# Optimization experiments

Hardware: AMD Instinct MI355X
Metric: run time of the kernel (lower is better)

The kernel has to match this reference:

```python
import jax, jax.numpy as jnp
import numpy as np

N_NODES = 100000
N_EDGES = 600000
D_IN = 128
D_HID = 128
D_OUT = 128


def setup_inputs() -> dict:
    key = jax.random.key(0)
    k = jax.random.split(key, 6)
    x = jax.random.normal(k[0], (N_NODES, D_IN), dtype=jnp.float32)
    edge_index = jax.random.randint(k[1], (2, N_EDGES), 0, N_NODES, dtype=jnp.int64)
    # GCNConv params: glorot-ish weights, zero-init biases (randn-scaled here)
    W1 = jax.random.normal(k[2], (D_IN, D_HID), dtype=jnp.float32) / np.sqrt(D_IN)
    b1 = jnp.zeros((D_HID,), dtype=jnp.float32)
    W2 = jax.random.normal(k[3], (D_HID, D_OUT), dtype=jnp.float32) / np.sqrt(D_HID)
    b2 = jnp.zeros((D_OUT,), dtype=jnp.float32)
    return {"x": x, "edge_index": edge_index, "W1": W1, "b1": b1, "W2": W2, "b2": b2}


def _gcn_conv(x, W, b, src, dst, deg_inv_sqrt, n_nodes):
    # PyG GCNConv: h = x @ W; out_i = sum_{j->i} d_j^{-1/2} d_i^{-1/2} h_j + b
    h = x @ W  # [N, Dout]
    norm = (deg_inv_sqrt[src] * deg_inv_sqrt[dst])[:, None]  # [E, 1]
    msg = h[src] * norm  # gather: [E, Dout]
    out = jax.ops.segment_sum(msg, dst, num_segments=n_nodes)  # scatter-add
    return out + b


def reference(x, edge_index, W1, b1, W2, b2):
    n = x.shape[0]
    # add self loops
    loops = jnp.arange(n, dtype=edge_index.dtype)
    src = jnp.concatenate([edge_index[0], loops])
    dst = jnp.concatenate([edge_index[1], loops])
    # symmetric normalization degrees (computed on dst, deg >= 1 due to self loops)
    deg = jax.ops.segment_sum(jnp.ones_like(dst, dtype=x.dtype), dst, num_segments=n)
    deg_inv_sqrt = jax.lax.rsqrt(deg)
    h = _gcn_conv(x, W1, b1, src, dst, deg_inv_sqrt, n)
    h = jax.nn.relu(h)  # dropout is identity in eval mode
    out = _gcn_conv(h, W2, b2, src, dst, deg_inv_sqrt, n)
    return out
```

## Files before the change

### kernel.cpp

```cpp
#include <hip/hip_runtime.h>

#define D 128

typedef __attribute__((ext_vector_type(8))) short bf16x8;
typedef __attribute__((ext_vector_type(4))) float f32x4;
typedef __attribute__((ext_vector_type(4))) unsigned u32x4;

__device__ inline unsigned short f2bf(float f) {
    unsigned u = __builtin_bit_cast(unsigned, f);
    u += 0x7FFFu + ((u >> 16) & 1u);
    return (unsigned short)(u >> 16);
}
__device__ inline float bf_lo(unsigned u) { return __builtin_bit_cast(float, u << 16); }
__device__ inline float bf_hi(unsigned u) { return __builtin_bit_cast(float, u & 0xFFFF0000u); }

__global__ __launch_bounds__(256) void k_pack_zero(const float* __restrict__ W1,
                                                   const float* __restrict__ W2,
                                                   unsigned short* __restrict__ wp,
                                                   int* __restrict__ counts, int n) {
    if (blockIdx.x < 16) {
        const int t = blockIdx.x * 256 + threadIdx.x;
        const float* W = (t < 2048) ? W1 : W2;
        const int tt = t & 2047;
        const int lane = tt & 63;
        const int frag = tt >> 6;
        const int ct = frag >> 2;
        const int kk = frag & 3;
        const int col16 = lane & 15;
        const int kgrp = lane >> 4;
        bf16x8 d;
#pragma unroll
        for (int e = 0; e < 8; ++e)
            d[e] = (short)f2bf(W[(kk * 32 + kgrp * 8 + e) * D + ct * 16 + col16]);
        *reinterpret_cast<bf16x8*>(wp + (size_t)t * 8) = d;
    } else {
        const int i = (blockIdx.x - 16) * 256 + threadIdx.x;
        if (i < n) counts[i] = 0;
    }
}

__global__ void k_hist_rank(const int* __restrict__ dst, int* __restrict__ counts,
                            int* __restrict__ rank, int nE) {
    int e4 = (blockIdx.x * blockDim.x + threadIdx.x) * 4;
    if (e4 + 4 <= nE) {
        const int4 d = *reinterpret_cast<const int4*>(dst + e4);
        int4 r;
        r.x = atomicAdd(&counts[d.x], 1);
        r.y = atomicAdd(&counts[d.y], 1);
        r.z = atomicAdd(&counts[d.z], 1);
        r.w = atomicAdd(&counts[d.w], 1);
        *reinterpret_cast<int4*>(rank + e4) = r;
    } else {
        for (int e = e4; e < nE; ++e) rank[e] = atomicAdd(&counts[dst[e]], 1);
    }
}

__global__ __launch_bounds__(256) void k_scan_part(const int* __restrict__ counts,
                                                   int* __restrict__ bsum,
                                                   float* __restrict__ dis, int n) {
    const int t = threadIdx.x;
    const int base = blockIdx.x * 1024 + t * 4;
    int4 c = make_int4(0, 0, 0, 0);
    if (base + 4 <= n) {
        c = *reinterpret_cast<const int4*>(counts + base);
        float4 dv;
        dv.x = rsqrtf((float)(c.x + 1));
        dv.y = rsqrtf((float)(c.y + 1));
        dv.z = rsqrtf((float)(c.z + 1));
        dv.w = rsqrtf((float)(c.w + 1));
        *reinterpret_cast<float4*>(dis + base) = dv;
    } else if (base < n) {
        int cc[4] = {0, 0, 0, 0};
        for (int k = 0; k < 4; ++k)
            if (base + k < n) {
                cc[k] = counts[base + k];
                dis[base + k] = rsqrtf((float)(cc[k] + 1));
            }
        c.x = cc[0]; c.y = cc[1]; c.z = cc[2]; c.w = cc[3];
    }
    __shared__ int red[256];
    red[t] = c.x + c.y + c.z + c.w;
    __syncthreads();
    for (int off = 128; off > 0; off >>= 1) {
        if (t < off) red[t] += red[t + off];
        __syncthreads();
    }
    if (t == 0) bsum[blockIdx.x] = red[0];
}

__global__ __launch_bounds__(256) void k_scan_final(const int* __restrict__ counts,
                                                    const int* __restrict__ bsum,
                                                    int* __restrict__ starts, int n, int nB) {
    __shared__ int sb[128];
    __shared__ int ts[256];
    const int t = threadIdx.x;
    const int b = blockIdx.x;

    if (t < 128) sb[t] = (t < nB) ? bsum[t] : 0;
    __syncthreads();
    for (int off = 1; off < 128; off <<= 1) {
        int add = (t < 128 && t >= off) ? sb[t - off] : 0;
        __syncthreads();
        if (t < 128) sb[t] += add;
        __syncthreads();
    }
    const int block_off = (b > 0) ? sb[b - 1] : 0;

    const int base = b * 1024 + t * 4;
    int4 c = make_int4(0, 0, 0, 0);
    if (base + 4 <= n) {
        c = *reinterpret_cast<const int4*>(counts + base);
    } else if (base < n) {
        if (base + 0 < n) c.x = counts[base + 0];
        if (base + 1 < n) c.y = counts[base + 1];
        if (base + 2 < n) c.z = counts[base + 2];
    }
    const int s = c.x + c.y + c.z + c.w;
    ts[t] = s;
    __syncthreads();
    for (int off = 1; off < 256; off <<= 1) {
        int add = (t >= off) ? ts[t - off] : 0;
        __syncthreads();
        ts[t] += add;
        __syncthreads();
    }
    int excl = block_off + ts[t] - s;

    int4 w;
    w.x = excl;
    w.y = w.x + c.x;
    w.z = w.y + c.y;
    w.w = w.z + c.z;
    if (base + 4 <= n) {
        *reinterpret_cast<int4*>(starts + base) = w;
    } else if (base < n) {
        if (base + 0 < n) starts[base + 0] = w.x;
        if (base + 1 < n) starts[base + 1] = w.y;
        if (base + 2 < n) starts[base + 2] = w.z;
    }
    if (b == 0 && t == 0) starts[n] = sb[nB - 1];
}

__global__ __launch_bounds__(256, 3) void k_scatter_gemm(const int* __restrict__ src,
                                                         const int* __restrict__ dst,
                                                         const int* __restrict__ rank,
                                                         const int* __restrict__ starts,
                                                         int* __restrict__ esrc, int nE, int nsc,
                                                         const float* __restrict__ X,
                                                         const unsigned short* __restrict__ wp,
                                                         const float* __restrict__ dis,
                                                         unsigned short* __restrict__ outbf,
                                                         int n) {
    __shared__ __align__(16) unsigned short At[64 * 128];
    if (blockIdx.x < nsc) {
        int e4 = (blockIdx.x * blockDim.x + threadIdx.x) * 4;
        if (e4 + 4 <= nE) {
            const int4 s = *reinterpret_cast<const int4*>(src + e4);
            const int4 d = *reinterpret_cast<const int4*>(dst + e4);
            const int4 r = *reinterpret_cast<const int4*>(rank + e4);
            esrc[starts[d.x] + r.x] = s.x;
            esrc[starts[d.y] + r.y] = s.y;
            esrc[starts[d.z] + r.z] = s.z;
            esrc[starts[d.w] + r.w] = s.w;
        } else {
            for (int e = e4; e < nE; ++e)
                esrc[starts[dst[e]] + rank[e]] = src[e];
        }
        return;
    }
    const int st = blockIdx.x - nsc;
    const int tid = threadIdx.x;
    const int lane = tid & 63;
    const int wv = tid >> 6;
    const int col16 = lane & 15;
    const int kgrp = lane >> 4;

    float4 pf[8];
#pragma unroll
    for (int c = 0; c < 4; ++c) {
        const int idx = c * 2048 + tid * 8;
        const int row = idx >> 7;
        const int col = idx & 127;
        int grow = st * 64 + row;
        if (grow >= n) grow = n - 1;
        const float4* p = reinterpret_cast<const float4*>(X + (size_t)grow * D + col);
        pf[2 * c] = p[0];
        pf[2 * c + 1] = p[1];
    }
#pragma unroll
    for (int c = 0; c < 4; ++c) {
        const int idx = c * 2048 + tid * 8;
        const int row = idx >> 7;
        const int col = idx & 127;
        const float4 f0 = pf[2 * c], f1 = pf[2 * c + 1];
        float v[8] = {f0.x, f0.y, f0.z, f0.w, f1.x, f1.y, f1.z, f1.w};
        bf16x8 d;
#pragma unroll
        for (int e = 0; e < 8; ++e) d[e] = (short)f2bf(v[e]);
        const int waddr = row * 128 + (col ^ ((row & 7) << 3));
        *reinterpret_cast<bf16x8*>(&At[waddr]) = d;
    }
    __syncthreads();

    bf16x8 a[4];
#pragma unroll
    for (int kk = 0; kk < 4; ++kk) {
        const int raddr = (wv * 16 + col16) * 128 +
                          ((kk * 32 + kgrp * 8) ^ ((col16 & 7) << 3));
        a[kk] = *reinterpret_cast<const bf16x8*>(&At[raddr]);
    }

    const int node = st * 64 + wv * 16 + col16;
    const float dn = (node < n) ? dis[node] : 0.0f;
    unsigned short* op = outbf + (size_t)node * D + kgrp * 4;

#pragma unroll
    for (int h = 0; h < 2; ++h) {
        bf16x8 bw[4][4];
#pragma unroll
        for (int c2 = 0; c2 < 4; ++c2)
#pragma unroll
            for (int kk = 0; kk < 4; ++kk)
                bw[c2][kk] = *reinterpret_cast<const bf16x8*>(
                        wp + (size_t)(((h * 4 + c2) * 4 + kk) * 64 + lane) * 8);

        f32x4 acc[4];
#pragma unroll
        for (int c2 = 0; c2 < 4; ++c2) acc[c2] = (f32x4){0.f, 0.f, 0.f, 0.f};
#pragma unroll
        for (int kk = 0; kk < 4; ++kk)
#pragma unroll
            for (int c2 = 0; c2 < 4; ++c2)
                acc[c2] = __builtin_amdgcn_mfma_f32_16x16x32_bf16(bw[c2][kk], a[kk], acc[c2], 0, 0, 0);

        if (node < n) {
#pragma unroll
            for (int c2 = 0; c2 < 4; ++c2) {
                uint2 w;
                w.x = (unsigned)f2bf(dn * acc[c2][0]) | ((unsigned)f2bf(dn * acc[c2][1]) << 16);
                w.y = (unsigned)f2bf(dn * acc[c2][2]) | ((unsigned)f2bf(dn * acc[c2][3]) << 16);
                *reinterpret_cast<uint2*>(op + (h * 4 + c2) * 16) = w;
            }
        }
    }
}

__device__ __forceinline__ void accum_chunk(const unsigned short* __restrict__ hs,
                                            int myedge, int cnt, int grp, int sub,
                                            float acc[8]) {
    auto row16 = [&](int s) -> u32x4 {
        return *reinterpret_cast<const u32x4*>(hs + (size_t)s * D + sub * 8);
    };
    for (int k = 0; k < cnt; k += 8) {
        u32x4 u[8];
#pragma unroll
        for (int q = 0; q < 8; ++q) {
            const int tq = min(k + q, cnt - 1);
            const int s = __shfl(myedge, (grp << 4) | tq);
            u[q] = row16(s);
        }
        const int rem = cnt - k;
#pragma unroll
        for (int q = 0; q < 8; ++q) {
            if (q < rem) {
#pragma unroll
                for (int e = 0; e < 4; ++e) {
                    acc[2 * e] += bf_lo(u[q][e]);
                    acc[2 * e + 1] += bf_hi(u[q][e]);
                }
            }
        }
    }
}

__global__ __launch_bounds__(128, 4) void k_gather_gemm(const unsigned short* __restrict__ hs,
                                                        const int* __restrict__ starts,
                                                        const int* __restrict__ esrc,
                                                        const float* __restrict__ dis,
                                                        const float* __restrict__ bias,
                                                        const unsigned short* __restrict__ wp,
                                                        unsigned short* __restrict__ outbf,
                                                        int n) {
    __shared__ __align__(16) unsigned short At[32 * 128];
    const int tid = threadIdx.x;
    const int lane = tid & 63;
    const int wv = tid >> 6;
    const int col16 = lane & 15;
    const int kgrp = lane >> 4;
    const int grp = lane >> 4;
    const int sub = lane & 15;
    const int st = blockIdx.x;

    const float4 bv0 = reinterpret_cast<const float4*>(bias)[sub * 2 + 0];
    const float4 bv1 = reinterpret_cast<const float4*>(bias)[sub * 2 + 1];

    int ic[4], beg[4], end[4], cnt0[4], my[4];
    float di[4];
    u32x4 selfrow[4];
#pragma unroll
    for (int p = 0; p < 4; ++p) {
        const int i = st * 32 + wv * 16 + p * 4 + grp;
        ic[p] = (i < n) ? i : (n - 1);
    }
#pragma unroll
    for (int p = 0; p < 4; ++p) {
        beg[p] = starts[ic[p]];
        end[p] = starts[ic[p] + 1];
        di[p] = dis[ic[p]];
        selfrow[p] = *reinterpret_cast<const u32x4*>(hs + (size_t)ic[p] * D + sub * 8);
    }
#pragma unroll
    for (int p = 0; p < 4; ++p) {
        cnt0[p] = min(end[p] - beg[p], 16);
        my[p] = (sub < cnt0[p]) ? esrc[beg[p] + sub] : 0;
    }

#pragma unroll
    for (int p = 0; p < 4; ++p) {
        float acc[8];
#pragma unroll
        for (int e = 0; e < 4; ++e) {
            acc[2 * e] = bf_lo(selfrow[p][e]);
            acc[2 * e + 1] = bf_hi(selfrow[p][e]);
        }
        if (cnt0[p] > 0) accum_chunk(hs, my[p], cnt0[p], grp, sub, acc);
        for (int j = beg[p] + 16; j < end[p]; j += 16) {
            const int cnt = min(end[p] - j, 16);
            const int me = (sub < cnt) ? esrc[j + sub] : 0;
            accum_chunk(hs, me, cnt, grp, sub, acc);
        }

        float o[8];
        o[0] = di[p] * acc[0] + bv0.x; o[1] = di[p] * acc[1] + bv0.y;
        o[2] = di[p] * acc[2] + bv0.z; o[3] = di[p] * acc[3] + bv0.w;
        o[4] = di[p] * acc[4] + bv1.x; o[5] = di[p] * acc[5] + bv1.y;
        o[6] = di[p] * acc[6] + bv1.z; o[7] = di[p] * acc[7] + bv1.w;

        u32x4 w;
#pragma unroll
        for (int e = 0; e < 4; ++e)
            w[e] = (unsigned)f2bf(fmaxf(o[2 * e], 0.0f)) |
                   ((unsigned)f2bf(fmaxf(o[2 * e + 1], 0.0f)) << 16);
        const int lrow = wv * 16 + p * 4 + grp;
        const int waddr = lrow * 128 + ((sub * 8) ^ ((lrow & 7) << 3));
        *reinterpret_cast<u32x4*>(&At[waddr]) = w;
    }
    __syncthreads();

    bf16x8 a[4];
#pragma unroll
    for (int kk = 0; kk < 4; ++kk) {
        const int raddr = (wv * 16 + col16) * 128 +
                          ((kk * 32 + kgrp * 8) ^ ((col16 & 7) << 3));
        a[kk] = *reinterpret_cast<const bf16x8*>(&At[raddr]);
    }

    const int node = st * 32 + wv * 16 + col16;
    const float dn = (node < n) ? dis[node] : 0.0f;
    unsigned short* op = outbf + (size_t)node * D + kgrp * 4;

#pragma unroll
    for (int h = 0; h < 2; ++h) {
        bf16x8 bw[4][4];
#pragma unroll
        for (int c2 = 0; c2 < 4; ++c2)
#pragma unroll
            for (int kk = 0; kk < 4; ++kk)
                bw[c2][kk] = *reinterpret_cast<const bf16x8*>(
                        wp + (size_t)(((h * 4 + c2) * 4 + kk) * 64 + lane) * 8);

        f32x4 acc2[4];
#pragma unroll
        for (int c2 = 0; c2 < 4; ++c2) acc2[c2] = (f32x4){0.f, 0.f, 0.f, 0.f};
#pragma unroll
        for (int kk = 0; kk < 4; ++kk)
#pragma unroll
            for (int c2 = 0; c2 < 4; ++c2)
                acc2[c2] = __builtin_amdgcn_mfma_f32_16x16x32_bf16(bw[c2][kk], a[kk], acc2[c2], 0, 0, 0);

        if (node < n) {
#pragma unroll
            for (int c2 = 0; c2 < 4; ++c2) {
                uint2 w;
                w.x = (unsigned)f2bf(dn * acc2[c2][0]) | ((unsigned)f2bf(dn * acc2[c2][1]) << 16);
                w.y = (unsigned)f2bf(dn * acc2[c2][2]) | ((unsigned)f2bf(dn * acc2[c2][3]) << 16);
                *reinterpret_cast<uint2*>(op + (h * 4 + c2) * 16) = w;
            }
        }
    }
}

__global__ __launch_bounds__(256) void k_gather_agg(const unsigned short* __restrict__ hs,
                                                    const int* __restrict__ starts,
                                                    const int* __restrict__ esrc,
                                                    const float* __restrict__ dis,
                                                    const float* __restrict__ b,
                                                    float* __restrict__ outv, int n) {
    const int lane = threadIdx.x & 63;
    const int wv = threadIdx.x >> 6;
    const int grp = lane >> 4;
    const int sub = lane & 15;
    const int i = (blockIdx.x * 4 + wv) * 4 + grp;
    const bool active = (i < n);
    const int ic = active ? i : (n - 1);

    const float di = dis[ic];
    const int beg = starts[ic];
    const int end = starts[ic + 1];

    float acc[8];
    {
        const u32x4 u = *reinterpret_cast<const u32x4*>(hs + (size_t)ic * D + sub * 8);
#pragma unroll
        for (int e = 0; e < 4; ++e) {
            acc[2 * e] = bf_lo(u[e]);
            acc[2 * e + 1] = bf_hi(u[e]);
        }
    }
    for (int j = beg; j < end; j += 16) {
        const int cnt = min(end - j, 16);
        const int me = (sub < cnt) ? esrc[j + sub] : 0;
        accum_chunk(hs, me, cnt, grp, sub, acc);
    }

    if (!active) return;

    const float4 bv0 = reinterpret_cast<const float4*>(b)[sub * 2 + 0];
    const float4 bv1 = reinterpret_cast<const float4*>(b)[sub * 2 + 1];
    float4* op = reinterpret_cast<float4*>(outv + (size_t)i * D + sub * 8);
    op[0] = make_float4(di * acc[0] + bv0.x, di * acc[1] + bv0.y,
                        di * acc[2] + bv0.z, di * acc[3] + bv0.w);
    op[1] = make_float4(di * acc[4] + bv1.x, di * acc[5] + bv1.y,
                        di * acc[6] + bv1.z, di * acc[7] + bv1.w);
}

extern "C" void kernel_launch(void* const* d_in, const int* in_sizes, int n_in,
                              void* d_out, int out_size, void* d_ws, size_t ws_size,
                              hipStream_t stream) {
    const float* x  = (const float*)d_in[0];
    const int*   ei = (const int*)d_in[1];
    const float* W1 = (const float*)d_in[2];
    const float* b1 = (const float*)d_in[3];
    const float* W2 = (const float*)d_in[4];
    const float* b2 = (const float*)d_in[5];
    float* out = (float*)d_out;

    const int n  = in_sizes[0] / D;
    const int nE = in_sizes[1] / 2;
    const int* src = ei;
    const int* dst = ei + nE;

    char* ws = (char*)d_ws;
    float*          dis    = (float*)(ws);
    int*            counts = (int*)(ws + (1ull  << 19));
    int*            starts = (int*)(ws + (2ull  << 19));
    int*            esrc   = (int*)(ws + (4ull  << 19));
    int*            bsum   = (int*)(ws + (6ull  << 20));
    unsigned short* hs_bf  = (unsigned short*)(ws + (8ull  << 20));
    int*            rank   = (int*)(ws + (34ull << 20));
    unsigned short* wp     = (unsigned short*)(ws + (37ull << 20));
    unsigned short* hs2_bf = (unsigned short*)(ws + (40ull << 20));

    unsigned short* wp1 = wp;
    unsigned short* wp2 = wp + 2048 * 8;

    const int B = 256;
    const int gn = (n + B - 1) / B;
    const int ge4 = (nE + B * 4 - 1) / (B * 4);
    const int nB = (n + 1023) / 1024;

    k_pack_zero<<<16 + gn, B, 0, stream>>>(W1, W2, wp, counts, n);

    k_hist_rank<<<ge4, B, 0, stream>>>(dst, counts, rank, nE);
    k_scan_part<<<nB, B, 0, stream>>>(counts, bsum, dis, n);
    k_scan_final<<<nB, B, 0, stream>>>(counts, bsum, starts, n, nB);

    const int nst = (n + 63) / 64;
    const int nst32 = (n + 31) / 32;
    const int agg_grid = (n + 15) / 16;

    k_scatter_gemm<<<ge4 + nst, B, 0, stream>>>(src, dst, rank, starts, esrc, nE, ge4,
                                                x, wp1, dis, hs_bf, n);
    k_gather_gemm<<<nst32, 128, 0, stream>>>(hs_bf, starts, esrc, dis, b1, wp2, hs2_bf, n);
    k_gather_agg<<<agg_grid, B, 0, stream>>>(hs2_bf, starts, esrc, dis, b2, out, n);
}
```

Baseline: 142.2 us.

## Fuse first GEMM with degree histogram and apply source norm during gather

After: 141.7 us. Within noise of the previous version (-0.4%).

```diff
diff --git a/kernel.cpp b/kernel.cpp
--- a/kernel.cpp
+++ b/kernel.cpp
@@ -39,19 +39,102 @@
     }
 }
 
-__global__ void k_hist_rank(const int* __restrict__ dst, int* __restrict__ counts,
-                            int* __restrict__ rank, int nE) {
-    int e4 = (blockIdx.x * blockDim.x + threadIdx.x) * 4;
-    if (e4 + 4 <= nE) {
-        const int4 d = *reinterpret_cast<const int4*>(dst + e4);
-        int4 r;
-        r.x = atomicAdd(&counts[d.x], 1);
-        r.y = atomicAdd(&counts[d.y], 1);
-        r.z = atomicAdd(&counts[d.z], 1);
-        r.w = atomicAdd(&counts[d.w], 1);
-        *reinterpret_cast<int4*>(rank + e4) = r;
-    } else {
-        for (int e = e4; e < nE; ++e) rank[e] = atomicAdd(&counts[dst[e]], 1);
+__global__ __launch_bounds__(256, 3) void k_hist_gemm(const int* __restrict__ dst,
+                                                      int* __restrict__ counts,
+                                                      int* __restrict__ rank, int nE, int nsc,
+                                                      const float* __restrict__ X,
+                                                      const unsigned short* __restrict__ wp,
+                                                      unsigned short* __restrict__ outbf,
+                                                      int n) {
+    __shared__ __align__(16) unsigned short At[64 * 128];
+    if (blockIdx.x < nsc) {
+        int e4 = (blockIdx.x * blockDim.x + threadIdx.x) * 4;
+        if (e4 + 4 <= nE) {
+            const int4 d = *reinterpret_cast<const int4*>(dst + e4);
+            int4 r;
+            r.x = atomicAdd(&counts[d.x], 1);
+            r.y = atomicAdd(&counts[d.y], 1);
+            r.z = atomicAdd(&counts[d.z], 1);
+            r.w = atomicAdd(&counts[d.w], 1);
+            *reinterpret_cast<int4*>(rank + e4) = r;
+        } else {
+            for (int e = e4; e < nE; ++e) rank[e] = atomicAdd(&counts[dst[e]], 1);
+        }
+        return;
+    }
+    const int st = blockIdx.x - nsc;
+    const int tid = threadIdx.x;
+    const int lane = tid & 63;
+    const int wv = tid >> 6;
+    const int col16 = lane & 15;
+    const int kgrp = lane >> 4;
+
+    float4 pf[8];
+#pragma unroll
+    for (int c = 0; c < 4; ++c) {
+        const int idx = c * 2048 + tid * 8;
+        const int row = idx >> 7;
+        const int col = idx & 127;
+        int grow = st * 64 + row;
+        if (grow >= n) grow = n - 1;
+        const float4* p = reinterpret_cast<const float4*>(X + (size_t)grow * D + col);
+        pf[2 * c] = p[0];
+        pf[2 * c + 1] = p[1];
+    }
+#pragma unroll
+    for (int c = 0; c < 4; ++c) {
+        const int idx = c * 2048 + tid * 8;
+        const int row = idx >> 7;
+        const int col = idx & 127;
+        const float4 f0 = pf[2 * c], f1 = pf[2 * c + 1];
+        float v[8] = {f0.x, f0.y, f0.z, f0.w, f1.x, f1.y, f1.z, f1.w};
+        bf16x8 d;
+#pragma unroll
+        for (int e = 0; e < 8; ++e) d[e] = (short)f2bf(v[e]);
+        const int waddr = row * 128 + (col ^ ((row & 7) << 3));
+        *reinterpret_cast<bf16x8*>(&At[waddr]) = d;
+    }
+    __syncthreads();
+
+    bf16x8 a[4];
+#pragma unroll
+    for (int kk = 0; kk < 4; ++kk) {
+        const int raddr = (wv * 16 + col16) * 128 +
+                          ((kk * 32 + kgrp * 8) ^ ((col16 & 7) << 3));
+        a[kk] = *reinterpret_cast<const bf16x8*>(&At[raddr]);
+    }
+
+    const int node = st * 64 + wv * 16 + col16;
+    unsigned short* op = outbf + (size_t)node * D + kgrp * 4;
+
+#pragma unroll
+    for (int h = 0; h < 2; ++h) {
+        bf16x8 bw[4][4];
+#pragma unroll
+        for (int c2 = 0; c2 < 4; ++c2)
+#pragma unroll
+            for (int kk = 0; kk < 4; ++kk)
+                bw[c2][kk] = *reinterpret_cast<const bf16x8*>(
+                        wp + (size_t)(((h * 4 + c2) * 4 + kk) * 64 + lane) * 8);
+
+        f32x4 acc[4];
+#pragma unroll
+        for (int c2 = 0; c2 < 4; ++c2) acc[c2] = (f32x4){0.f, 0.f, 0.f, 0.f};
+#pragma unroll
+        for (int kk = 0; kk < 4; ++kk)
+#pragma unroll
+            for (int c2 = 0; c2 < 4; ++c2)
+                acc[c2] = __builtin_amdgcn_mfma_f32_16x16x32_bf16(bw[c2][kk], a[kk], acc[c2], 0, 0, 0);
+
+        if (node < n) {
+#pragma unroll
+            for (int c2 = 0; c2 < 4; ++c2) {
+                uint2 w;
+                w.x = (unsigned)f2bf(acc[c2][0]) | ((unsigned)f2bf(acc[c2][1]) << 16);
+                w.y = (unsigned)f2bf(acc[c2][2]) | ((unsigned)f2bf(acc[c2][3]) << 16);
+                *reinterpret_cast<uint2*>(op + (h * 4 + c2) * 16) = w;
+            }
+        }
     }
 }
 
@@ -141,107 +224,21 @@
     if (b == 0 && t == 0) starts[n] = sb[nB - 1];
 }
 
-__global__ __launch_bounds__(256, 3) void k_scatter_gemm(const int* __restrict__ src,
-                                                         const int* __restrict__ dst,
-                                                         const int* __restrict__ rank,
-                                                         const int* __restrict__ starts,
-                                                         int* __restrict__ esrc, int nE, int nsc,
-                                                         const float* __restrict__ X,
-                                                         const unsigned short* __restrict__ wp,
-                                                         const float* __restrict__ dis,
-                                                         unsigned short* __restrict__ outbf,
-                                                         int n) {
-    __shared__ __align__(16) unsigned short At[64 * 128];
-    if (blockIdx.x < nsc) {
-        int e4 = (blockIdx.x * blockDim.x + threadIdx.x) * 4;
-        if (e4 + 4 <= nE) {
-            const int4 s = *reinterpret_cast<const int4*>(src + e4);
-            const int4 d = *reinterpret_cast<const int4*>(dst + e4);
-            const int4 r = *reinterpret_cast<const int4*>(rank + e4);
-            esrc[starts[d.x] + r.x] = s.x;
-            esrc[starts[d.y] + r.y] = s.y;
-            esrc[starts[d.z] + r.z] = s.z;
-            esrc[starts[d.w] + r.w] = s.w;
-        } else {
-            for (int e = e4; e < nE; ++e)
-                esrc[starts[dst[e]] + rank[e]] = src[e];
-        }
-        return;
-    }
-    const int st = blockIdx.x - nsc;
-    const int tid = threadIdx.x;
-    const int lane = tid & 63;
-    const int wv = tid >> 6;
-    const int col16 = lane & 15;
-    const int kgrp = lane >> 4;
-
-    float4 pf[8];
-#pragma unroll
-    for (int c = 0; c < 4; ++c) {
-        const int idx = c * 2048 + tid * 8;
-        const int row = idx >> 7;
-        const int col = idx & 127;
-        int grow = st * 64 + row;
-        if (grow >= n) grow = n - 1;
-        const float4* p = reinterpret_cast<const float4*>(X + (size_t)grow * D + col);
-        pf[2 * c] = p[0];
-        pf[2 * c + 1] = p[1];
-    }
-#pragma unroll
-    for (int c = 0; c < 4; ++c) {
-        const int idx = c * 2048 + tid * 8;
-        const int row = idx >> 7;
-        const int col = idx & 127;
-        const float4 f0 = pf[2 * c], f1 = pf[2 * c + 1];
-        float v[8] = {f0.x, f0.y, f0.z, f0.w, f1.x, f1.y, f1.z, f1.w};
-        bf16x8 d;
-#pragma unroll
-        for (int e = 0; e < 8; ++e) d[e] = (short)f2bf(v[e]);
-        const int waddr = row * 128 + (col ^ ((row & 7) << 3));
-        *reinterpret_cast<bf16x8*>(&At[waddr]) = d;
-    }
-    __syncthreads();
-
-    bf16x8 a[4];
-#pragma unroll
-    for (int kk = 0; kk < 4; ++kk) {
-        const int raddr = (wv * 16 + col16) * 128 +
-                          ((kk * 32 + kgrp * 8) ^ ((col16 & 7) << 3));
-        a[kk] = *reinterpret_cast<const bf16x8*>(&At[raddr]);
-    }
-
-    const int node = st * 64 + wv * 16 + col16;
-    const float dn = (node < n) ? dis[node] : 0.0f;
-    unsigned short* op = outbf + (size_t)node * D + kgrp * 4;
-
-#pragma unroll
-    for (int h = 0; h < 2; ++h) {
-        bf16x8 bw[4][4];
-#pragma unroll
-        for (int c2 = 0; c2 < 4; ++c2)
-#pragma unroll
-            for (int kk = 0; kk < 4; ++kk)
-                bw[c2][kk] = *reinterpret_cast<const bf16x8*>(
-                        wp + (size_t)(((h * 4 + c2) * 4 + kk) * 64 + lane) * 8);
-
-        f32x4 acc[4];
-#pragma unroll
-        for (int c2 = 0; c2 < 4; ++c2) acc[c2] = (f32x4){0.f, 0.f, 0.f, 0.f};
-#pragma unroll
-        for (int kk = 0; kk < 4; ++kk)
-#pragma unroll
-            for (int c2 = 0; c2 < 4; ++c2)
-                acc[c2] = __builtin_amdgcn_mfma_f32_16x16x32_bf16(bw[c2][kk], a[kk], acc[c2], 0, 0, 0);
-
-        if (node < n) {
-#pragma unroll
-            for (int c2 = 0; c2 < 4; ++c2) {
-                uint2 w;
-                w.x = (unsigned)f2bf(dn * acc[c2][0]) | ((unsigned)f2bf(dn * acc[c2][1]) << 16);
-                w.y = (unsigned)f2bf(dn * acc[c2][2]) | ((unsigned)f2bf(dn * acc[c2][3]) << 16);
-                *reinterpret_cast<uint2*>(op + (h * 4 + c2) * 16) = w;
-            }
-        }
+__global__ void k_scatter_nr(const int* __restrict__ src, const int* __restrict__ dst,
+                             const int* __restrict__ rank, const int* __restrict__ starts,
+                             int* __restrict__ esrc, int nE) {
+    int e4 = (blockIdx.x * blockDim.x + threadIdx.x) * 4;
+    if (e4 + 4 <= nE) {
+        const int4 s = *reinterpret_cast<const int4*>(src + e4);
+        const int4 d = *reinterpret_cast<const int4*>(dst + e4);
+        const int4 r = *reinterpret_cast<const int4*>(rank + e4);
+        esrc[starts[d.x] + r.x] = s.x;
+        esrc[starts[d.y] + r.y] = s.y;
+        esrc[starts[d.z] + r.z] = s.z;
+        esrc[starts[d.w] + r.w] = s.w;
+    } else {
+        for (int e = e4; e < nE; ++e)
+            esrc[starts[dst[e]] + rank[e]] = src[e];
     }
 }
 
@@ -267,6 +264,37 @@
                 for (int e = 0; e < 4; ++e) {
                     acc[2 * e] += bf_lo(u[q][e]);
                     acc[2 * e + 1] += bf_hi(u[q][e]);
+                }
+            }
+        }
+    }
+}
+
+__device__ __forceinline__ void accum_chunk_w(const unsigned short* __restrict__ hs,
+                                              int myedge, float myw, int cnt, int grp, int sub,
+                                              float acc[8]) {
+    auto row16 = [&](int s) -> u32x4 {
+        return *reinterpret_cast<const u32x4*>(hs + (size_t)s * D + sub * 8);
+    };
+    for (int k = 0; k < cnt; k += 8) {
+        u32x4 u[8];
+        float w[8];
+#pragma unroll
+        for (int q = 0; q < 8; ++q) {
+            const int tq = min(k + q, cnt - 1);
+            const int sl = (grp << 4) | tq;
+            const int s = __shfl(myedge, sl);
+            w[q] = __shfl(myw, sl);
+            u[q] = row16(s);
+        }
+        const int rem = cnt - k;
+#pragma unroll
+        for (int q = 0; q < 8; ++q) {
+            if (q < rem) {
+#pragma unroll
+                for (int e = 0; e < 4; ++e) {
+                    acc[2 * e] += w[q] * bf_lo(u[q][e]);
+                    acc[2 * e + 1] += w[q] * bf_hi(u[q][e]);
                 }
             }
         }
@@ -295,7 +323,7 @@
     const float4 bv1 = reinterpret_cast<const float4*>(bias)[sub * 2 + 1];
 
     int ic[4], beg[4], end[4], cnt0[4], my[4];
-    float di[4];
+    float di[4], wd[4];
     u32x4 selfrow[4];
 #pragma unroll
     for (int p = 0; p < 4; ++p) {
@@ -314,20 +342,24 @@
         cnt0[p] = min(end[p] - beg[p], 16);
         my[p] = (sub < cnt0[p]) ? esrc[beg[p] + sub] : 0;
     }
+#pragma unroll
+    for (int p = 0; p < 4; ++p)
+        wd[p] = (sub < cnt0[p]) ? dis[my[p]] : 0.0f;
 
 #pragma unroll
     for (int p = 0; p < 4; ++p) {
         float acc[8];
 #pragma unroll
         for (int e = 0; e < 4; ++e) {
-            acc[2 * e] = bf_lo(selfrow[p][e]);
-            acc[2 * e + 1] = bf_hi(selfrow[p][e]);
-        }
-        if (cnt0[p] > 0) accum_chunk(hs, my[p], cnt0[p], grp, sub, acc);
+            acc[2 * e] = di[p] * bf_lo(selfrow[p][e]);
+            acc[2 * e + 1] = di[p] * bf_hi(selfrow[p][e]);
+        }
+        if (cnt0[p] > 0) accum_chunk_w(hs, my[p], wd[p], cnt0[p], grp, sub, acc);
         for (int j = beg[p] + 16; j < end[p]; j += 16) {
             const int cnt = min(end[p] - j, 16);
             const int me = (sub < cnt) ? esrc[j + sub] : 0;
-            accum_chunk(hs, me, cnt, grp, sub, acc);
+            const float mw = (sub < cnt) ? dis[me] : 0.0f;
+            accum_chunk_w(hs, me, mw, cnt, grp, sub, acc);
         }
 
         float o[8];
@@ -469,18 +501,18 @@
     const int ge4 = (nE + B * 4 - 1) / (B * 4);
     const int nB = (n + 1023) / 1024;
 
-    k_pack_zero<<<16 + gn, B, 0, stream>>>(W1, W2, wp, counts, n);
-
-    k_hist_rank<<<ge4, B, 0, stream>>>(dst, counts, rank, nE);
-    k_scan_part<<<nB, B, 0, stream>>>(counts, bsum, dis, n);
-    k_scan_final<<<nB, B, 0, stream>>>(counts, bsum, starts, n, nB);
-
     const int nst = (n + 63) / 64;
     const int nst32 = (n + 31) / 32;
     const int agg_grid = (n + 15) / 16;
 
-    k_scatter_gemm<<<ge4 + nst, B, 0, stream>>>(src, dst, rank, starts, esrc, nE, ge4,
-                                                x, wp1, dis, hs_bf, n);
+    k_pack_zero<<<16 + gn, B, 0, stream>>>(W1, W2, wp, counts, n);
+
+    k_hist_gemm<<<ge4 + nst, B, 0, stream>>>(dst, counts, rank, nE, ge4,
+                                             x, wp1, hs_bf, n);
+    k_scan_part<<<nB, B, 0, stream>>>(counts, bsum, dis, n);
+    k_scan_final<<<nB, B, 0, stream>>>(counts, bsum, starts, n, nB);
+    k_scatter_nr<<<ge4, B, 0, stream>>>(src, dst, rank, starts, esrc, nE);
+
     k_gather_gemm<<<nst32, 128, 0, stream>>>(hs_bf, starts, esrc, dis, b1, wp2, hs2_bf, n);
     k_gather_agg<<<agg_grid, B, 0, stream>>>(hs2_bf, starts, esrc, dis, b2, out, n);
 }
```
